# Optimization experiments

Measured on AMD Instinct MI355X. Metric: run time of the kernel, lower is better.

## Reference

```python
import jax, jax.numpy as jnp
import numpy as np

SCALE = 64.0
MARGIN = 0.5
ALPHA = 1.2
SIGMA = 2.0
THRESH = float(np.cos(np.pi - MARGIN))
MM = float(np.sin(np.pi - MARGIN) * MARGIN)
IN_F, OUT_F, BATCH = 512, 100000, 512


def setup_inputs() -> dict:
    key = jax.random.key(0)
    k1, k2, k3 = jax.random.split(key, 3)
    x = jax.random.normal(k1, (BATCH, IN_F), dtype=jnp.float32)
    label = jax.random.randint(k2, (BATCH,), 0, OUT_F, dtype=jnp.int64 if jax.config.read('jax_enable_x64') else jnp.int32)
    stdv = 1.0 / np.sqrt(IN_F)
    weight = jax.random.uniform(k3, (OUT_F, IN_F), dtype=jnp.float32, minval=-stdv, maxval=stdv)
    return {"input": x, "label": label, "weight": weight}


def reference(input, label, weight):
    # row-normalize embeddings and class weights
    ex = input / jnp.linalg.norm(input, axis=1, keepdims=True)
    ew = weight / jnp.linalg.norm(weight, axis=1, keepdims=True)
    cos = jnp.einsum('bd,cd->bc', ex, ew)  # [B, C]

    b = jnp.arange(cos.shape[0])
    cos_lb = cos[b, label]  # [B] cosine at the true class
    # arcface margin: cos(theta + m) above thresh, linear fallback below
    target = jnp.where(cos_lb > THRESH,
                       jnp.cos(jnp.arccos(cos_lb) + MARGIN),
                       cos_lb - MM)  # [B]

    # negative reweighting: gaussian around the margined target (detached)
    t_scale = ALPHA * jnp.exp(-jnp.square(cos - target[:, None]) / SIGMA)
    t_scale = jax.lax.stop_gradient(t_scale)

    onehot = jax.nn.one_hot(label, cos.shape[1], dtype=cos.dtype)  # a_scale; c_scale = 1 - onehot
    logits = SCALE * (onehot * target[:, None]
                      + (1.0 - onehot) * (t_scale * cos + t_scale - 1.0))
    return logits
```

## Files before the change

### kernel.cpp

```cpp
#include <hip/hip_runtime.h>
#include <hip/hip_bf16.h>

typedef unsigned short ushort_t;
typedef unsigned int uint_t;

typedef __attribute__((ext_vector_type(8))) short short8;
typedef __attribute__((ext_vector_type(4))) float f32x4;

#define BATCH 512
#define DK    512
#define CTOT  100000
#define CPAD  100032
#define BN    32
#define BNF   64
#define THRESH_C (-0.8775825618903728f)
#define MM_C     (0.2397127693021015f)

static __device__ __forceinline__ ushort_t f2bf(float f) {
    union { float f; uint_t u; } v; v.f = f;
    return (ushort_t)((v.u + 0x7FFFu + ((v.u >> 16) & 1u)) >> 16);
}

__global__ __launch_bounds__(256) void arc_prep(
    const float* __restrict__ x, const int* __restrict__ label,
    const float* __restrict__ w, float* __restrict__ target,
    ushort_t* __restrict__ exbF)
{
    const int b = blockIdx.x;
    const int t = threadIdx.x;
    __shared__ float red[8];

    const float2 xv = ((const float2*)(x + (size_t)b * DK))[t];
    float ss = xv.x * xv.x + xv.y * xv.y;
    #pragma unroll
    for (int o = 32; o; o >>= 1) ss += __shfl_xor(ss, o);
    if ((t & 63) == 0) red[t >> 6] = ss;
    __syncthreads();
    const float ssx = red[0] + red[1] + red[2] + red[3];
    const float rnx = 1.0f / sqrtf(ssx);

    {
        const int k = 2 * t;
        const int ko = k >> 5;
        const int qk = (k >> 3) & 3;
        const int kj = k & 7;
        const size_t F = (size_t)(b >> 4) * 8192 + (size_t)ko * 512
                       + (size_t)qk * 128 + (size_t)(b & 15) * 8 + kj;
        ushort2 e;
        e.x = f2bf(xv.x * rnx);
        e.y = f2bf(xv.y * rnx);
        *(ushort2*)(exbF + F) = e;
    }

    const int lb = label[b];
    const float2 wv = ((const float2*)(w + (size_t)lb * DK))[t];
    float ssw = wv.x * wv.x + wv.y * wv.y;
    float dot = xv.x * wv.x + xv.y * wv.y;
    #pragma unroll
    for (int o = 32; o; o >>= 1) { ssw += __shfl_xor(ssw, o); dot += __shfl_xor(dot, o); }
    __syncthreads();
    if ((t & 63) == 0) { red[t >> 6] = ssw; red[4 + (t >> 6)] = dot; }
    __syncthreads();
    if (t == 0) {
        const float sw = red[0] + red[1] + red[2] + red[3];
        const float dt = red[4] + red[5] + red[6] + red[7];
        float cl = dt * rnx / sqrtf(sw);
        cl = fminf(fmaxf(cl, -1.0f), 1.0f);
        const float tg = (cl > THRESH_C) ? cosf(acosf(cl) + 0.5f) : (cl - MM_C);
        target[b] = tg;
    }
}

__global__ __launch_bounds__(256) void arc_wcvt(
    const float* __restrict__ w, ushort_t* __restrict__ wbF,
    float* __restrict__ rnw)
{
    const int rb  = blockIdx.x;
    const int t   = threadIdx.x;
    const int r   = t >> 4;
    const int c16 = t & 15;
    const int row = rb * 16 + r;
    const bool valid = (row < CTOT);
    const float* wrow = w + (size_t)row * DK;
    ushort_t* fbase = wbF + (size_t)rb * 8192 + (size_t)r * 8;

    float ss = 0.0f;
    #pragma unroll
    for (int i = 0; i < 4; ++i) {
        const int c = i * 128 + c16 * 8;
        float4 q0 = make_float4(0.f, 0.f, 0.f, 0.f);
        float4 q1 = q0;
        if (valid) {
            q0 = *(const float4*)(wrow + c);
            q1 = *(const float4*)(wrow + c + 4);
        }
        ss += q0.x * q0.x + q0.y * q0.y + q0.z * q0.z + q0.w * q0.w
            + q1.x * q1.x + q1.y * q1.y + q1.z * q1.z + q1.w * q1.w;
        uint4 p;
        p.x = (uint_t)f2bf(q0.x) | ((uint_t)f2bf(q0.y) << 16);
        p.y = (uint_t)f2bf(q0.z) | ((uint_t)f2bf(q0.w) << 16);
        p.z = (uint_t)f2bf(q1.x) | ((uint_t)f2bf(q1.y) << 16);
        p.w = (uint_t)f2bf(q1.z) | ((uint_t)f2bf(q1.w) << 16);
        const int ko = c >> 5;
        const int qk = (c >> 3) & 3;
        *(uint4*)(fbase + ko * 512 + qk * 128) = p;
    }
    ss += __shfl_xor(ss, 1);
    ss += __shfl_xor(ss, 2);
    ss += __shfl_xor(ss, 4);
    ss += __shfl_xor(ss, 8);
    if (c16 == 0) rnw[row] = valid ? (1.0f / sqrtf(ss)) : 0.0f;
}

__global__ __launch_bounds__(512, 4) void arc_main_ff(
    const ushort_t* __restrict__ exbF, const ushort_t* __restrict__ wbF,
    const float* __restrict__ rnw, const int* __restrict__ label,
    const float* __restrict__ target, float* __restrict__ out)
{
    const int t    = threadIdx.x;
    const int lane = t & 63;
    const int wid  = t >> 6;
    const int tile = blockIdx.x;
    const int c0   = tile * BNF;
    const int colq = lane & 15;
    const int qk   = lane >> 4;

    const ushort_t* abase = exbF + (size_t)(wid * 4) * 8192 + (size_t)lane * 8;
    const ushort_t* bbase = wbF + (size_t)(tile * 4) * 8192 + (size_t)lane * 8;

    f32x4 acc[4][4];
    #pragma unroll
    for (int i = 0; i < 4; ++i)
        #pragma unroll
        for (int j = 0; j < 4; ++j)
            acc[i][j] = (f32x4){0.f, 0.f, 0.f, 0.f};

    #pragma unroll 4
    for (int ko = 0; ko < 16; ++ko) {
        short8 bfr[4];
        #pragma unroll
        for (int nt = 0; nt < 4; ++nt)
            bfr[nt] = *(const short8*)(bbase + (size_t)nt * 8192 + ko * 512);
        #pragma unroll
        for (int mt = 0; mt < 4; ++mt) {
            const short8 afr = *(const short8*)(abase + (size_t)mt * 8192 + ko * 512);
            #pragma unroll
            for (int nt = 0; nt < 4; ++nt)
                acc[mt][nt] = __builtin_amdgcn_mfma_f32_16x16x32_bf16(afr, bfr[nt], acc[mt][nt], 0, 0, 0);
        }
    }

    float rn[4];
    #pragma unroll
    for (int nt = 0; nt < 4; ++nt) rn[nt] = rnw[c0 + nt * 16 + colq];

    const int m0 = wid * 64;

#define EPILOGUE(GUARD)                                                        \
    _Pragma("unroll")                                                          \
    for (int mt = 0; mt < 4; ++mt) {                                           \
        _Pragma("unroll")                                                      \
        for (int rr = 0; rr < 4; ++rr) {                                       \
            const int row = m0 + mt * 16 + qk * 4 + rr;                        \
            const float tg = target[row];                                      \
            const int   lb = label[row];                                       \
            float* orow = out + (size_t)row * CTOT + c0;                       \
            _Pragma("unroll")                                                  \
            for (int nt = 0; nt < 4; ++nt) {                                   \
                const int cc = c0 + nt * 16 + colq;                            \
                if (GUARD && cc >= CTOT) continue;                             \
                const float cosv = acc[mt][nt][rr] * rn[nt];                   \
                const float d  = cosv - tg;                                    \
                const float ts = 1.2f * __expf(d * d * -0.5f);                 \
                const float v  = (cc == lb) ? 64.0f * tg                       \
                                            : 64.0f * (ts * cosv + ts - 1.0f); \
                orow[nt * 16 + colq] = v;                                      \
            }                                                                  \
        }                                                                      \
    }

    if (c0 + BNF <= CTOT) {
        EPILOGUE(false)
    } else {
        EPILOGUE(true)
    }
#undef EPILOGUE
}

__global__ __launch_bounds__(512, 8) void arc_main_lds(
    const ushort_t* __restrict__ exbF, const float* __restrict__ w,
    const int* __restrict__ label, const float* __restrict__ target,
    float* __restrict__ out)
{
    __shared__ ushort_t Bs[BN * DK];

    const int t    = threadIdx.x;
    const int lane = t & 63;
    const int wid  = t >> 6;
    const int c0   = blockIdx.x * BN;

    const int br  = t >> 4;
    const int bj  = t & 15;
    const float* wrow = w + (size_t)(c0 + br) * DK;
    const int s3 = br & 7;
    float bsq = 0.0f;
    #pragma unroll
    for (int i = 0; i < 8; ++i) {
        const int c = i * 64 + bj * 4;
        const float4 q = *(const float4*)(wrow + c);
        bsq += q.x * q.x + q.y * q.y + q.z * q.z + q.w * q.w;
        uint2 p;
        p.x = (uint_t)f2bf(q.x) | ((uint_t)f2bf(q.y) << 16);
        p.y = (uint_t)f2bf(q.z) | ((uint_t)f2bf(q.w) << 16);
        const int k16 = c >> 3;
        const int sw  = k16 ^ s3;
        *(uint2*)&Bs[br * DK + sw * 8 + (bj & 1) * 4] = p;
    }
    bsq += __shfl_xor(bsq, 1);
    bsq += __shfl_xor(bsq, 2);
    bsq += __shfl_xor(bsq, 4);
    bsq += __shfl_xor(bsq, 8);
    __syncthreads();

    const int m0   = wid * 64;
    const int colq = lane & 15;
    const int qk   = lane >> 4;
    const int bs3  = colq & 7;
    const ushort_t* abase = exbF + (size_t)(wid * 4) * 8192 + (size_t)lane * 8;

    f32x4 acc[4][2];
    #pragma unroll
    for (int i = 0; i < 4; ++i)
        #pragma unroll
        for (int j = 0; j < 2; ++j)
            acc[i][j] = (f32x4){0.f, 0.f, 0.f, 0.f};

    #pragma unroll 2
    for (int ko = 0; ko < 16; ++ko) {
        short8 bfr[2];
        #pragma unroll
        for (int nt = 0; nt < 2; ++nt) {
            const int idx = (nt * 16 + colq) * DK + (((ko << 2) | qk) ^ bs3) * 8;
            bfr[nt] = *(const short8*)&Bs[idx];
        }
        #pragma unroll
        for (int mt = 0; mt < 4; ++mt) {
            const short8 afr = *(const short8*)(abase + (size_t)mt * 8192 + ko * 512);
            acc[mt][0] = __builtin_amdgcn_mfma_f32_16x16x32_bf16(afr, bfr[0], acc[mt][0], 0, 0, 0);
            acc[mt][1] = __builtin_amdgcn_mfma_f32_16x16x32_bf16(afr, bfr[1], acc[mt][1], 0, 0, 0);
        }
    }

    __syncthreads();
    if (bj == 0) ((float*)Bs)[br] = 1.0f / sqrtf(bsq);
    __syncthreads();
    float rn[2];
    rn[0] = ((float*)Bs)[colq];
    rn[1] = ((float*)Bs)[16 + colq];

    #pragma unroll
    for (int mt = 0; mt < 4; ++mt) {
        #pragma unroll
        for (int rr = 0; rr < 4; ++rr) {
            const int row = m0 + mt * 16 + qk * 4 + rr;
            const float tg = target[row];
            const int   lb = label[row];
            float* orow = out + (size_t)row * CTOT + c0;
            #pragma unroll
            for (int nt = 0; nt < 2; ++nt) {
                const int cc = c0 + nt * 16 + colq;
                const float cosv = acc[mt][nt][rr] * rn[nt];
                const float d  = cosv - tg;
                const float ts = 1.2f * __expf(d * d * -0.5f);
                const float v  = (cc == lb) ? 64.0f * tg
                                            : 64.0f * (ts * cosv + ts - 1.0f);
                orow[nt * 16 + colq] = v;
            }
        }
    }
}

extern "C" void kernel_launch(void* const* d_in, const int* in_sizes, int n_in,
                              void* d_out, int out_size, void* d_ws, size_t ws_size,
                              hipStream_t stream) {
    const float* x     = (const float*)d_in[0];
    const int*   label = (const int*)d_in[1];
    const float* w     = (const float*)d_in[2];
    float* out = (float*)d_out;

    float*    target = (float*)d_ws;
    ushort_t* exbF   = (ushort_t*)((char*)d_ws + 2048);
    float*    rnw    = (float*)((char*)d_ws + 526336);
    ushort_t* wbF    = (ushort_t*)((char*)d_ws + 926720);
    const size_t WS_NEED = 926720 + (size_t)CPAD * DK * 2;

    arc_prep<<<512, 256, 0, stream>>>(x, label, w, target, exbF);

    if (ws_size >= WS_NEED) {
        arc_wcvt<<<CPAD / 16, 256, 0, stream>>>(w, wbF, rnw);
        arc_main_ff<<<CPAD / BNF, 512, 0, stream>>>(exbF, wbF, rnw, label, target, out);
    } else {
        arc_main_lds<<<CTOT / BN, 512, 0, stream>>>(exbF, w, label, target, out);
    }
}
```

Measured before the change: 452.2 us.

## Stage B tile in LDS and transpose epilogue for vectorized nontemporal stores

The FF main kernel now copies its whole 64-column bf16 weight tile into shared memory once per block instead of having all eight waves read it from global memory separately. The epilogue writes each 16-row chunk of results into a padded per-wave LDS buffer and reads it back transposed, so every lane issues a 16-byte nontemporal store of four consecutive columns rather than scattered 4-byte stores. The aim is less redundant global traffic and more efficient writes of the 200MB output. The cost is 64KB of LDS per block, which may limit occupancy below the declared four blocks per CU, plus extra barriers and LDS round trips.

```diff
diff --git a/kernel.cpp b/kernel.cpp
--- a/kernel.cpp
+++ b/kernel.cpp
@@ -117,6 +117,8 @@
     const float* __restrict__ rnw, const int* __restrict__ label,
     const float* __restrict__ target, float* __restrict__ out)
 {
+    __shared__ ushort_t Bs[4 * 8192];
+
     const int t    = threadIdx.x;
     const int lane = t & 63;
     const int wid  = t >> 6;
@@ -125,8 +127,15 @@
     const int colq = lane & 15;
     const int qk   = lane >> 4;
 
+    {
+        const uint4* gB = (const uint4*)(wbF + (size_t)tile * 4 * 8192);
+        uint4* lB = (uint4*)Bs;
+        #pragma unroll
+        for (int i = 0; i < 8; ++i)
+            lB[i * 512 + t] = gB[i * 512 + t];
+    }
+
     const ushort_t* abase = exbF + (size_t)(wid * 4) * 8192 + (size_t)lane * 8;
-    const ushort_t* bbase = wbF + (size_t)(tile * 4) * 8192 + (size_t)lane * 8;
 
     f32x4 acc[4][4];
     #pragma unroll
@@ -135,56 +144,73 @@
         for (int j = 0; j < 4; ++j)
             acc[i][j] = (f32x4){0.f, 0.f, 0.f, 0.f};
 
-    #pragma unroll 4
+    __syncthreads();
+
+    const ushort_t* bbase = Bs + (size_t)lane * 8;
+    #pragma unroll 2
     for (int ko = 0; ko < 16; ++ko) {
-        short8 bfr[4];
+        short8 bfr[4], afr[4];
         #pragma unroll
         for (int nt = 0; nt < 4; ++nt)
-            bfr[nt] = *(const short8*)(bbase + (size_t)nt * 8192 + ko * 512);
-        #pragma unroll
-        for (int mt = 0; mt < 4; ++mt) {
-            const short8 afr = *(const short8*)(abase + (size_t)mt * 8192 + ko * 512);
+            bfr[nt] = *(const short8*)(bbase + nt * 8192 + ko * 512);
+        #pragma unroll
+        for (int mt = 0; mt < 4; ++mt)
+            afr[mt] = *(const short8*)(abase + (size_t)mt * 8192 + ko * 512);
+        #pragma unroll
+        for (int mt = 0; mt < 4; ++mt)
             #pragma unroll
             for (int nt = 0; nt < 4; ++nt)
-                acc[mt][nt] = __builtin_amdgcn_mfma_f32_16x16x32_bf16(afr, bfr[nt], acc[mt][nt], 0, 0, 0);
-        }
+                acc[mt][nt] = __builtin_amdgcn_mfma_f32_16x16x32_bf16(
+                    afr[mt], bfr[nt], acc[mt][nt], 0, 0, 0);
     }
 
     float rn[4];
     #pragma unroll
     for (int nt = 0; nt < 4; ++nt) rn[nt] = rnw[c0 + nt * 16 + colq];
 
-    const int m0 = wid * 64;
-
-#define EPILOGUE(GUARD)                                                        \
-    _Pragma("unroll")                                                          \
-    for (int mt = 0; mt < 4; ++mt) {                                           \
-        _Pragma("unroll")                                                      \
-        for (int rr = 0; rr < 4; ++rr) {                                       \
-            const int row = m0 + mt * 16 + qk * 4 + rr;                        \
-            const float tg = target[row];                                      \
-            const int   lb = label[row];                                       \
-            float* orow = out + (size_t)row * CTOT + c0;                       \
-            _Pragma("unroll")                                                  \
-            for (int nt = 0; nt < 4; ++nt) {                                   \
-                const int cc = c0 + nt * 16 + colq;                            \
-                if (GUARD && cc >= CTOT) continue;                             \
-                const float cosv = acc[mt][nt][rr] * rn[nt];                   \
-                const float d  = cosv - tg;                                    \
-                const float ts = 1.2f * __expf(d * d * -0.5f);                 \
-                const float v  = (cc == lb) ? 64.0f * tg                       \
-                                            : 64.0f * (ts * cosv + ts - 1.0f); \
-                orow[nt * 16 + colq] = v;                                      \
-            }                                                                  \
-        }                                                                      \
-    }
-
-    if (c0 + BNF <= CTOT) {
-        EPILOGUE(false)
-    } else {
-        EPILOGUE(true)
-    }
-#undef EPILOGUE
+    __syncthreads();
+
+    float* Ts = (float*)Bs + wid * (16 * 67);
+
+    const int  m0   = wid * 64;
+    const bool full = (c0 + BNF <= CTOT);
+
+    #pragma unroll
+    for (int mt = 0; mt < 4; ++mt) {
+        #pragma unroll
+        for (int rr = 0; rr < 4; ++rr) {
+            const int row = m0 + mt * 16 + qk * 4 + rr;
+            const float tg = target[row];
+            const int   lb = label[row];
+            #pragma unroll
+            for (int nt = 0; nt < 4; ++nt) {
+                const int cc = c0 + nt * 16 + colq;
+                const float cosv = acc[mt][nt][rr] * rn[nt];
+                const float d  = cosv - tg;
+                const float ts = 1.2f * __expf(d * d * -0.5f);
+                const float v  = (cc == lb) ? 64.0f * tg
+                                            : 64.0f * (ts * cosv + ts - 1.0f);
+                Ts[(qk * 4 + rr) * 67 + nt * 16 + colq] = v;
+            }
+        }
+        asm volatile("s_waitcnt lgkmcnt(0)" ::: "memory");
+
+        #pragma unroll
+        for (int i = 0; i < 4; ++i) {
+            const int r16 = i * 4 + qk;
+            const int row = m0 + mt * 16 + r16;
+            const int cc4 = 4 * colq;
+            f32x4 v;
+            v.x = Ts[r16 * 67 + cc4 + 0];
+            v.y = Ts[r16 * 67 + cc4 + 1];
+            v.z = Ts[r16 * 67 + cc4 + 2];
+            v.w = Ts[r16 * 67 + cc4 + 3];
+            if (full || (c0 + cc4 < CTOT))
+                __builtin_nontemporal_store(
+                    v, (f32x4*)(out + (size_t)row * CTOT + c0 + cc4));
+        }
+        asm volatile("s_waitcnt lgkmcnt(0)" ::: "memory");
+    }
 }
 
 __global__ __launch_bounds__(512, 8) void arc_main_lds(
```

After: 416.9 us. -7.8%, faster.
